# Performance work log

Measured on AMD Instinct MI355X. Metric: run time of the kernel, lower is better.

Reference implementation:

```python
import jax, jax.numpy as jnp
import numpy as np

B, D_IN, EMB = 8192, 4000, 96
H0, H1 = 2048, 1024
NB, NC, OPT = 8, 8, 32
NE = NB * NC  # 64 experts (total contests)


def setup_inputs() -> dict:
    key = jax.random.key(0)
    ks = jax.random.split(key, 10)
    scale = lambda fan_in: jnp.sqrt(2.0 / fan_in)  # kaiming_normal-ish
    return {
        "inputs": jax.random.normal(ks[0], (B, D_IN), dtype=jnp.float32),
        "emb_table": jax.random.normal(ks[1], (NE, EMB), dtype=jnp.float32) * scale(EMB),
        "W0": jax.random.normal(ks[2], (D_IN + EMB, H0), dtype=jnp.float32) * scale(D_IN + EMB),
        "b0": jnp.zeros((H0,), dtype=jnp.float32),
        "W1": jax.random.normal(ks[3], (H0, H1), dtype=jnp.float32) * scale(H0),
        "b1": jnp.zeros((H1,), dtype=jnp.float32),
        "We": jax.random.normal(ks[4], (NE, H1, OPT), dtype=jnp.float32) * scale(H1),
        "be": jnp.zeros((NE, OPT), dtype=jnp.float32),
        "ballot_number": jax.random.randint(ks[5], (B,), 0, NB, dtype=jnp.int32),
        "contest_number": jax.random.randint(ks[6], (B,), 0, NC, dtype=jnp.int32),
        "batches": B,
    }


def reference(inputs, emb_table, W0, b0, W1, b1, We, be,
              ballot_number, contest_number, batches):
    # flat expert index per sample: index_of[ballot][contest] with equal-size ballots
    expert = ballot_number * NC + contest_number                  # [B]
    x = inputs.reshape(batches, -1)                               # [B, D_IN]
    emb = emb_table[expert]                                       # [B, EMB] (gather)
    h = jnp.concatenate([emb, x], axis=1)                         # [B, D_IN+EMB]
    h = jax.nn.relu(h @ W0 + b0)                                  # fc0 (dropout = id at eval)
    h = jax.nn.relu(h @ W1 + b1)                                  # fc1
    # per-sample routed linear: gather expert weights, batched matvec
    out = jnp.einsum("bd,bdo->bo", h, We[expert]) + be[expert]    # [B, OPT]
    return jax.nn.sigmoid(out)
```

## Files before the change

### kernel.cpp

```cpp
#include <hip/hip_runtime.h>
#include <math.h>

typedef __attribute__((ext_vector_type(8))) short short8;
typedef __attribute__((ext_vector_type(4))) float f32x4;

#define B_SZ 8192
#define D_INN 4000
#define EMBD 96
#define H0D 2048
#define H1D 1024
#define KDIM 4096

#define MFMA_BF16 __builtin_amdgcn_mfma_f32_16x16x32_bf16

__device__ __forceinline__ unsigned short f2bf(float f) {
  union { float f; unsigned u; } v; v.f = f;
  unsigned r = v.u + 0x7FFFu + ((v.u >> 16) & 1u);
  return (unsigned short)(r >> 16);
}
__device__ __forceinline__ float bf2f(unsigned short h) {
  union { unsigned u; float f; } v; v.u = ((unsigned)h) << 16;
  return v.f;
}
__device__ __forceinline__ void gld_lds16(const void* g, void* l) {
  __builtin_amdgcn_global_load_lds(
      (const __attribute__((address_space(1))) unsigned int*)g,
      (__attribute__((address_space(3))) unsigned int*)l, 16, 0, 0);
}

__global__ __launch_bounds__(256) void transpose_cvt(
    const float* __restrict__ in, unsigned short* __restrict__ out, int R, int C) {
  __shared__ float tile[32][33];
  int c0 = blockIdx.x * 32, r0 = blockIdx.y * 32;
  int tc = threadIdx.x & 31, tr = threadIdx.x >> 5;
#pragma unroll
  for (int i = 0; i < 4; ++i) {
    int r = tr + i * 8;
    tile[r][tc] = in[(size_t)(r0 + r) * C + (c0 + tc)];
  }
  __syncthreads();
#pragma unroll
  for (int i = 0; i < 4; ++i) {
    int rr = tr + i * 8;
    out[(size_t)(c0 + rr) * R + (r0 + tc)] = f2bf(tile[tc][rr]);
  }
}

__global__ __launch_bounds__(256) void transpose_cvt_we(
    const float* __restrict__ in, unsigned short* __restrict__ out) {
  __shared__ float tile[32][33];
  const int e = blockIdx.y, r0 = blockIdx.x * 32;
  const float* src = in + (size_t)e * 32768;
  unsigned short* dst = out + (size_t)e * 32768;
  int tc = threadIdx.x & 31, tr = threadIdx.x >> 5;
#pragma unroll
  for (int i = 0; i < 4; ++i) {
    int r = tr + i * 8;
    tile[r][tc] = src[(size_t)(r0 + r) * 32 + tc];
  }
  __syncthreads();
#pragma unroll
  for (int i = 0; i < 4; ++i) {
    int rr = tr + i * 8;
    dst[(size_t)rr * H1D + r0 + tc] = f2bf(tile[tc][rr]);
  }
}

__global__ __launch_bounds__(256) void build_A(
    const float* __restrict__ inputs, const float* __restrict__ emb,
    const int* __restrict__ ballot, const int* __restrict__ contest,
    unsigned short* __restrict__ A) {
  int gid = blockIdx.x * 256 + threadIdx.x;
  int b = gid >> 9, c = gid & 511;
  const float* src;
  if (c < EMBD / 8) {
    int e = ballot[b] * 8 + contest[b];
    src = emb + (size_t)e * EMBD + c * 8;
  } else {
    src = inputs + (size_t)b * D_INN + (c - EMBD / 8) * 8;
  }
  float4 v0 = *(const float4*)src;
  float4 v1 = *(const float4*)(src + 4);
  unsigned short r[8];
  r[0] = f2bf(v0.x); r[1] = f2bf(v0.y); r[2] = f2bf(v0.z); r[3] = f2bf(v0.w);
  r[4] = f2bf(v1.x); r[5] = f2bf(v1.y); r[6] = f2bf(v1.z); r[7] = f2bf(v1.w);
  *reinterpret_cast<short8*>(A + (size_t)b * KDIM + c * 8) =
      *reinterpret_cast<const short8*>(r);
}

template <int MREP>
__global__ __launch_bounds__(512, 2) void gemm_nt_pipe(
    const unsigned short* __restrict__ A, const unsigned short* __restrict__ Bt,
    const float* __restrict__ bias, unsigned short* __restrict__ C,
    int K, int N, int NBN) {
  constexpr int BM  = MREP * 32;
  constexpr int AI  = MREP / 4;
  constexpr int ASH = BM * 32;
  constexpr int MH  = MREP / 2;
  __shared__ unsigned short lds[3 * ASH + 3 * 8192];

  const int tid = threadIdx.x;
  const int w = tid >> 6, l = tid & 63;
  const int lr = l & 15, kg = l >> 4;
  const int wm = w >> 2, wn = w & 3;

  int swz = (blockIdx.x & 7) * ((int)gridDim.x >> 3) + ((int)blockIdx.x >> 3);
  const int bm = swz / NBN, bn = swz - bm * NBN;
  const int NT = K >> 5;

  const int rg = l >> 2;
  const int sl = ((l & 3) ^ ((l >> 3) & 3)) * 8;
  const unsigned short* ga[AI];
#pragma unroll
  for (int i = 0; i < AI; ++i)
    ga[i] = A + (size_t)(bm * BM + (i * 8 + w) * 16 + rg) * K + sl;
  const unsigned short* gb0 = Bt + (size_t)(bn * 256 + w * 16 + rg) * K + sl;
  const unsigned short* gb1 = gb0 + (size_t)128 * K;

  const int xo = (kg ^ ((lr >> 1) & 3)) << 4;
  const int aoff = (wm * (MREP * 16) + lr) * 64 + xo;
  const int boff = (wn * 64 + lr) * 64 + xo;

  f32x4 acc[MREP][4] = {};

  auto stageA = [&](int t, int rbuf) {
    unsigned short* la = lds + rbuf * ASH + w * 512;
    const int ko = t * 32;
#pragma unroll
    for (int i = 0; i < AI; ++i) gld_lds16(ga[i] + ko, la + i * 4096);
  };
  auto stageB = [&](int t, int rbuf) {
    unsigned short* lb = lds + 3 * ASH + rbuf * 8192 + w * 512;
    const int ko = t * 32;
    gld_lds16(gb0 + ko, lb);
    gld_lds16(gb1 + ko, lb + 4096);
  };

#define WAIT_VM_STEADY() do { \
    if constexpr (AI == 2) asm volatile("s_waitcnt vmcnt(4)" ::: "memory"); \
    else                   asm volatile("s_waitcnt vmcnt(3)" ::: "memory"); \
  } while (0)

  stageA(0, 0); stageB(0, 0);
  stageA(1, 1); stageB(1, 1);
  WAIT_VM_STEADY();
  __builtin_amdgcn_s_barrier();

  int rb = 0;
  for (int t = 0; t < NT; ++t) {
    int rb2 = rb + 2; if (rb2 >= 3) rb2 -= 3;
    const char* pa = (const char*)lds + rb * (ASH * 2) + aoff;
    const char* pb = (const char*)lds + 3 * (ASH * 2) + rb * 16384 + boff;

    short8 a0[MH], bfr[4];
#pragma unroll
    for (int mi = 0; mi < MH; ++mi) a0[mi] = *(const short8*)(pa + mi * 1024);
#pragma unroll
    for (int ni = 0; ni < 4; ++ni)  bfr[ni] = *(const short8*)(pb + ni * 1024);
    if (t + 2 < NT) stageA(t + 2, rb2);
    asm volatile("s_waitcnt lgkmcnt(0)" ::: "memory");
    __builtin_amdgcn_s_barrier();
    __builtin_amdgcn_s_setprio(1);
#pragma unroll
    for (int mi = 0; mi < MH; ++mi)
#pragma unroll
      for (int ni = 0; ni < 4; ++ni)
        acc[mi][ni] = MFMA_BF16(a0[mi], bfr[ni], acc[mi][ni], 0, 0, 0);
    __builtin_amdgcn_s_setprio(0);

    short8 a1[MH];
#pragma unroll
    for (int mi = 0; mi < MH; ++mi) a1[mi] = *(const short8*)(pa + (MH + mi) * 1024);
    if (t + 2 < NT) {
      stageB(t + 2, rb2);
      asm volatile("s_waitcnt lgkmcnt(0)" ::: "memory");
      WAIT_VM_STEADY();
      __builtin_amdgcn_s_barrier();
    } else if (t + 1 < NT) {
      asm volatile("s_waitcnt lgkmcnt(0)" ::: "memory");
      asm volatile("s_waitcnt vmcnt(0)" ::: "memory");
      __builtin_amdgcn_s_barrier();
    } else {
      asm volatile("s_waitcnt lgkmcnt(0)" ::: "memory");
    }
    __builtin_amdgcn_s_setprio(1);
#pragma unroll
    for (int mi = 0; mi < MH; ++mi)
#pragma unroll
      for (int ni = 0; ni < 4; ++ni)
        acc[MH + mi][ni] = MFMA_BF16(a1[mi], bfr[ni], acc[MH + mi][ni], 0, 0, 0);
    __builtin_amdgcn_s_setprio(0);

    rb = rb + 1; if (rb >= 3) rb = 0;
  }

#pragma unroll
  for (int mi = 0; mi < MREP; ++mi) {
    const int row0 = bm * BM + wm * (MREP * 16) + mi * 16 + kg * 4;
#pragma unroll
    for (int ni = 0; ni < 4; ++ni) {
      const int col = bn * 256 + wn * 64 + ni * 16 + lr;
      const float bv = bias[col];
#pragma unroll
      for (int j = 0; j < 4; ++j) {
        float v = acc[mi][ni][j] + bv;
        v = v > 0.f ? v : 0.f;
        C[(size_t)(row0 + j) * N + col] = f2bf(v);
      }
    }
  }
#undef WAIT_VM_STEADY
}

__global__ __launch_bounds__(256) void expert_head_mfma(
    const unsigned short* __restrict__ h1, const unsigned short* __restrict__ Wet,
    const float* __restrict__ be, const int* __restrict__ ballot,
    const int* __restrict__ contest, float* __restrict__ out) {
  const int e = blockIdx.x;
  __shared__ unsigned short sidx[1024];
  __shared__ int scnt;
  if (threadIdx.x == 0) scnt = 0;
  __syncthreads();
  for (int i = threadIdx.x; i < B_SZ; i += 256)
    if (ballot[i] * 8 + contest[i] == e) {
      int p = atomicAdd(&scnt, 1);
      if (p < 1024) sidx[p] = (unsigned short)i;
    }
  __syncthreads();
  const int cnt = min(scnt, 1024);
  const int w = threadIdx.x >> 6, l = threadIdx.x & 63;
  const int lr = l & 15, kg = l >> 4;
  const unsigned short* wbase = Wet + (size_t)e * 32768;
  for (int c0 = w * 32; c0 < cnt; c0 += 128) {
    const int ns = min(32, cnt - c0);
    f32x4 acc[2][2] = {};
    int ridx[2];
#pragma unroll
    for (int mi = 0; mi < 2; ++mi) {
      int rr = mi * 16 + lr;
      ridx[mi] = sidx[c0 + (rr < ns ? rr : 0)];
    }
#pragma unroll 4
    for (int kk = 0; kk < 32; ++kk) {
      short8 a0 = *(const short8*)(h1 + (size_t)ridx[0] * H1D + kk * 32 + kg * 8);
      short8 a1 = *(const short8*)(h1 + (size_t)ridx[1] * H1D + kk * 32 + kg * 8);
      short8 b0 = *(const short8*)(wbase + (size_t)lr * H1D + kk * 32 + kg * 8);
      short8 b1 = *(const short8*)(wbase + (size_t)(16 + lr) * H1D + kk * 32 + kg * 8);
      acc[0][0] = MFMA_BF16(a0, b0, acc[0][0], 0, 0, 0);
      acc[0][1] = MFMA_BF16(a0, b1, acc[0][1], 0, 0, 0);
      acc[1][0] = MFMA_BF16(a1, b0, acc[1][0], 0, 0, 0);
      acc[1][1] = MFMA_BF16(a1, b1, acc[1][1], 0, 0, 0);
    }
#pragma unroll
    for (int mi = 0; mi < 2; ++mi)
#pragma unroll
      for (int ni = 0; ni < 2; ++ni)
#pragma unroll
        for (int j = 0; j < 4; ++j) {
          int row = mi * 16 + kg * 4 + j;
          int col = ni * 16 + lr;
          if (row < ns) {
            float x = acc[mi][ni][j] + be[e * 32 + col];
            out[(size_t)sidx[c0 + row] * 32 + col] = 1.f / (1.f + expf(-x));
          }
        }
  }
}

extern "C" void kernel_launch(void* const* d_in, const int* in_sizes, int n_in,
                              void* d_out, int out_size, void* d_ws, size_t ws_size,
                              hipStream_t stream) {
  const float* inputs = (const float*)d_in[0];
  const float* emb    = (const float*)d_in[1];
  const float* W0     = (const float*)d_in[2];
  const float* b0     = (const float*)d_in[3];
  const float* W1     = (const float*)d_in[4];
  const float* b1     = (const float*)d_in[5];
  const float* We     = (const float*)d_in[6];
  const float* be     = (const float*)d_in[7];
  const int* ballot   = (const int*)d_in[8];
  const int* contest  = (const int*)d_in[9];
  float* out = (float*)d_out;

  char* ws = (char*)d_ws;
  unsigned short* A   = (unsigned short*)(ws);
  unsigned short* W0t = (unsigned short*)(ws + 67108864);
  unsigned short* h0  = (unsigned short*)(ws + 83886080);
  unsigned short* W1t = (unsigned short*)(ws + 117440512);
  unsigned short* h1  = (unsigned short*)(ws + 121634816);
  unsigned short* Wet = (unsigned short*)(ws);

  dim3 blk(256);
  transpose_cvt<<<dim3(H0D / 32, KDIM / 32, 1), blk, 0, stream>>>(W0, W0t, KDIM, H0D);
  transpose_cvt<<<dim3(H1D / 32, H0D / 32, 1), blk, 0, stream>>>(W1, W1t, H0D, H1D);
  build_A<<<dim3(B_SZ * 512 / 256), blk, 0, stream>>>(inputs, emb, ballot, contest, A);
  gemm_nt_pipe<8><<<dim3((B_SZ / 256) * (H0D / 256)), dim3(512), 0, stream>>>(
      A, W0t, b0, h0, KDIM, H0D, H0D / 256);
  transpose_cvt_we<<<dim3(32, 64), blk, 0, stream>>>(We, Wet);
  gemm_nt_pipe<4><<<dim3((B_SZ / 128) * (H1D / 256)), dim3(512), 0, stream>>>(
      h0, W1t, b1, h1, H0D, H1D, H1D / 256);
  expert_head_mfma<<<dim3(64), blk, 0, stream>>>(h1, Wet, be, ballot, contest, out);
}
```

Baseline: 243.2 us.

## Replace fc0 GEMM with 16-wave 256x256 tile kernel using triple-buffered LDS

Adds a new GEMM kernel for the first layer that runs 1024 threads (16 waves) per block on a 256x256 output tile, with K-step 32 and a three-slot LDS ring for A and B. Global-to-LDS loads are split into separate A and B stages interleaved with two halves of the MFMA work, and s_setprio raises priority around the MFMA bursts. This aims to improve latency hiding and MFMA utilization for the dominant 8192x2048x4096 GEMM, at the cost of one block per CU and higher register pressure per thread.

```diff
diff --git a/kernel.cpp b/kernel.cpp
--- a/kernel.cpp
+++ b/kernel.cpp
@@ -86,6 +86,111 @@
   r[4] = f2bf(v1.x); r[5] = f2bf(v1.y); r[6] = f2bf(v1.z); r[7] = f2bf(v1.w);
   *reinterpret_cast<short8*>(A + (size_t)b * KDIM + c * 8) =
       *reinterpret_cast<const short8*>(r);
+}
+
+template <int K>
+__global__ __launch_bounds__(1024) void gemm_nt_16w(
+    const unsigned short* __restrict__ A, const unsigned short* __restrict__ Bt,
+    const float* __restrict__ bias, unsigned short* __restrict__ C,
+    int N, int NBN) {
+  constexpr int SLOT = 16384;
+  __shared__ char lds[6 * SLOT];
+
+  const int tid = threadIdx.x;
+  const int w = tid >> 6, l = tid & 63;
+  const int lr = l & 15, kg = l >> 4;
+  const int wm = w >> 2, wn = w & 3;
+
+  int swz = (blockIdx.x & 7) * ((int)gridDim.x >> 3) + ((int)blockIdx.x >> 3);
+  const int bm = swz / NBN, bn = swz - bm * NBN;
+  const int NT = K >> 5;
+
+  const int srow = tid >> 2;
+  const int swzsl = (tid & 3) ^ ((srow >> 1) & 3);
+  const unsigned short* gaB = A + (size_t)(bm * 256 + srow) * K + swzsl * 8;
+  const unsigned short* gbB = Bt + (size_t)(bn * 256 + srow) * K + swzsl * 8;
+
+  const int xo = (kg ^ ((lr >> 1) & 3)) << 4;
+  const int aoff = (wm * 64 + lr) * 64 + xo;
+  const int boff = (wn * 64 + lr) * 64 + xo;
+
+  f32x4 acc[4][4] = {};
+
+  auto stageA = [&](int t, int rbuf) {
+    gld_lds16(gaB + t * 32, lds + rbuf * SLOT + tid * 16);
+  };
+  auto stageB = [&](int t, int rbuf) {
+    gld_lds16(gbB + t * 32, lds + 3 * SLOT + rbuf * SLOT + tid * 16);
+  };
+
+  stageA(0, 0); stageB(0, 0);
+  stageA(1, 1); stageB(1, 1);
+  asm volatile("s_waitcnt vmcnt(2)" ::: "memory");
+  __builtin_amdgcn_s_barrier();
+
+  int rb = 0;
+  for (int t = 0; t < NT; ++t) {
+    int rb2 = rb + 2; if (rb2 >= 3) rb2 -= 3;
+    const char* pa = lds + rb * SLOT + aoff;
+    const char* pb = lds + 3 * SLOT + rb * SLOT + boff;
+
+    short8 a0[2], bfr[4];
+#pragma unroll
+    for (int mi = 0; mi < 2; ++mi) a0[mi] = *(const short8*)(pa + mi * 1024);
+#pragma unroll
+    for (int ni = 0; ni < 4; ++ni) bfr[ni] = *(const short8*)(pb + ni * 1024);
+    if (t + 2 < NT) stageA(t + 2, rb2);
+    asm volatile("s_waitcnt lgkmcnt(0)" ::: "memory");
+    __builtin_amdgcn_s_barrier();
+    __builtin_amdgcn_s_setprio(1);
+#pragma unroll
+    for (int mi = 0; mi < 2; ++mi)
+#pragma unroll
+      for (int ni = 0; ni < 4; ++ni)
+        acc[mi][ni] = MFMA_BF16(a0[mi], bfr[ni], acc[mi][ni], 0, 0, 0);
+    __builtin_amdgcn_s_setprio(0);
+
+    short8 a1[2];
+#pragma unroll
+    for (int mi = 0; mi < 2; ++mi) a1[mi] = *(const short8*)(pa + (2 + mi) * 1024);
+    if (t + 2 < NT) {
+      stageB(t + 2, rb2);
+      asm volatile("s_waitcnt lgkmcnt(0)" ::: "memory");
+      asm volatile("s_waitcnt vmcnt(2)" ::: "memory");
+      __builtin_amdgcn_s_barrier();
+    } else if (t + 1 < NT) {
+      asm volatile("s_waitcnt lgkmcnt(0)" ::: "memory");
+      asm volatile("s_waitcnt vmcnt(0)" ::: "memory");
+      __builtin_amdgcn_s_barrier();
+    } else {
+      asm volatile("s_waitcnt lgkmcnt(0)" ::: "memory");
+    }
+    __builtin_amdgcn_s_setprio(1);
+#pragma unroll
+    for (int mi = 0; mi < 2; ++mi)
+#pragma unroll
+      for (int ni = 0; ni < 4; ++ni)
+        acc[2 + mi][ni] = MFMA_BF16(a1[mi], bfr[ni], acc[2 + mi][ni], 0, 0, 0);
+    __builtin_amdgcn_s_setprio(0);
+
+    rb = rb + 1; if (rb >= 3) rb = 0;
+  }
+
+#pragma unroll
+  for (int mi = 0; mi < 4; ++mi) {
+    const int row0 = bm * 256 + wm * 64 + mi * 16 + kg * 4;
+#pragma unroll
+    for (int ni = 0; ni < 4; ++ni) {
+      const int col = bn * 256 + wn * 64 + ni * 16 + lr;
+      const float bv = bias[col];
+#pragma unroll
+      for (int j = 0; j < 4; ++j) {
+        float v = acc[mi][ni][j] + bv;
+        v = v > 0.f ? v : 0.f;
+        C[(size_t)(row0 + j) * N + col] = f2bf(v);
+      }
+    }
+  }
 }
 
 template <int MREP>
@@ -294,8 +399,7 @@
   transpose_cvt<<<dim3(H0D / 32, KDIM / 32, 1), blk, 0, stream>>>(W0, W0t, KDIM, H0D);
   transpose_cvt<<<dim3(H1D / 32, H0D / 32, 1), blk, 0, stream>>>(W1, W1t, H0D, H1D);
   build_A<<<dim3(B_SZ * 512 / 256), blk, 0, stream>>>(inputs, emb, ballot, contest, A);
-  gemm_nt_pipe<8><<<dim3((B_SZ / 256) * (H0D / 256)), dim3(512), 0, stream>>>(
-      A, W0t, b0, h0, KDIM, H0D, H0D / 256);
+  gemm_nt_16w<KDIM><<<dim3(256), dim3(1024), 0, stream>>>(A, W0t, b0, h0, H0D, H0D / 256);
   transpose_cvt_we<<<dim3(32, 64), blk, 0, stream>>>(We, Wet);
   gemm_nt_pipe<4><<<dim3((B_SZ / 128) * (H1D / 256)), dim3(512), 0, stream>>>(
       h0, W1t, b1, h1, H0D, H1D, H1D / 256);
```

Result: no change. 242.8 us (-0.2%).
